# Kernel optimization log

Hardware: AMD Instinct MI355X
Metric: run time of the kernel (lower is better)

The kernel has to match this reference:

```python
import jax, jax.numpy as jnp
import numpy as np

B, C, H, W = 8, 512, 32, 32
NUM_HEADS = 8
HEAD_DIM = C // NUM_HEADS


def setup_inputs() -> dict:
    key = jax.random.key(0)
    k1, k2, k3 = jax.random.split(key, 3)
    query = jax.random.normal(k1, (B, C, H, W), dtype=jnp.float32)
    key_value = jax.random.normal(k2, (B, C, H, W), dtype=jnp.float32)
    # Linear(dim, 3*dim): store as [C, 3C] so y = x @ W + b
    W_qkv = jax.random.normal(k3, (C, 3 * C), dtype=jnp.float32) * (C ** -0.5)
    b_qkv = jnp.zeros((3 * C,), dtype=jnp.float32)
    return {"query": query, "key_value": key_value, "W_qkv": W_qkv, "b_qkv": b_qkv}


def reference(query, key_value, W_qkv, b_qkv):
    Bb, Cc, Hh, Ww = query.shape
    seq = Hh * Ww
    scale = HEAD_DIM ** -0.5

    # [B, C, H, W] -> [B, S, C]
    q_seq = query.reshape(Bb, Cc, seq).transpose(0, 2, 1)
    kv_seq = key_value.reshape(Bb, Cc, seq).transpose(0, 2, 1)

    # Original calls full qkv_proj and slices; math == projecting with sliced weights.
    q = q_seq @ W_qkv[:, :Cc] + b_qkv[:Cc]
    k = kv_seq @ W_qkv[:, Cc:2 * Cc] + b_qkv[Cc:2 * Cc]
    v = kv_seq @ W_qkv[:, 2 * Cc:] + b_qkv[2 * Cc:]

    def heads(x):  # [B, S, C] -> [B, nH, S, hd]
        return x.reshape(Bb, seq, NUM_HEADS, HEAD_DIM).transpose(0, 2, 1, 3)

    q, k, v = heads(q), heads(k), heads(v)
    attn = jnp.einsum('bhqd,bhkd->bhqk', q, k) * scale
    attn = jax.nn.softmax(attn, axis=-1)  # dropout: identity in eval
    out = jnp.einsum('bhqk,bhkd->bhqd', attn, v)
    # [B, nH, S, hd] -> [B, S, C] -> [B, C, H, W]
    out = out.transpose(0, 2, 1, 3).reshape(Bb, seq, Cc)
    return out.transpose(0, 2, 1).reshape(Bb, Cc, Hh, Ww)
```

## Files before the change

### kernel.cpp

```cpp
#include <hip/hip_runtime.h>
#include <hip/hip_bf16.h>

using short4v = __attribute__((ext_vector_type(4))) short;
using short8  = __attribute__((ext_vector_type(8))) short;
using uint2v  = __attribute__((ext_vector_type(2))) unsigned int;
using f32x4   = __attribute__((ext_vector_type(4))) float;

static constexpr int CDIM = 512;
static constexpr float KSCALE = 0.125f * 1.44269504088896341f;

__device__ __forceinline__ short f2bf(float f) {
  unsigned u = __builtin_bit_cast(unsigned, f);
  u = (u + 0x7fffu + ((u >> 16) & 1u)) >> 16;
  return (short)(unsigned short)u;
}
__device__ __forceinline__ unsigned pack_bf16(float a, float b) {
  return (unsigned)(unsigned short)f2bf(a) | ((unsigned)(unsigned short)f2bf(b) << 16);
}

#define GLOAD_LDS16(gp, lp)                                                              \
  __builtin_amdgcn_global_load_lds((const __attribute__((address_space(1))) void*)(gp),  \
                                   (__attribute__((address_space(3))) void*)(lp), 16, 0, 0)
#define MFMA16(a, b, c) __builtin_amdgcn_mfma_f32_16x16x32_bf16((a), (b), (c), 0, 0, 0)
#define WAIT_LGKM0() __builtin_amdgcn_s_waitcnt(0xc07f)

__global__ __launch_bounds__(256) void prep_transpose(const float* __restrict__ query,
                                                      const float* __restrict__ keyv,
                                                      const float* __restrict__ Wqkv,
                                                      short* __restrict__ Xq_t,
                                                      short* __restrict__ Xkv_t,
                                                      short* __restrict__ W_t) {
  __shared__ float tile[64 * 65];
  const int id = blockIdx.x;
  const float* s; short* d; int R, C, r0, c0;
  if (id < 2048) {
    const int which = id >> 10;
    int rem = id & 1023;
    const int b = rem >> 7; rem &= 127;
    R = 512; C = 1024;
    s = (which ? keyv : query) + (size_t)b * 512 * 1024;
    d = (which ? Xkv_t : Xq_t) + (size_t)b * 512 * 1024;
    r0 = (rem >> 4) * 64; c0 = (rem & 15) * 64;
  } else {
    const int rem = id - 2048;
    R = 512; C = 1536; s = Wqkv; d = W_t;
    r0 = (rem / 24) * 64; c0 = (rem % 24) * 64;
  }
  const int t  = threadIdx.x;
  const int rr = t >> 4;
  const int c4 = (t & 15) * 4;
#pragma unroll
  for (int i = 0; i < 4; ++i) {
    const int r = rr + i * 16;
    f32x4 v = *(const f32x4*)(s + (size_t)(r0 + r) * C + c0 + c4);
#pragma unroll
    for (int j = 0; j < 4; ++j) tile[(c4 + j) * 65 + r] = v[j];
  }
  __syncthreads();
  const int r8 = (t & 7) * 8;
#pragma unroll
  for (int i = 0; i < 2; ++i) {
    const int c = (t >> 3) + i * 32;
    short8 pk;
#pragma unroll
    for (int j = 0; j < 8; ++j) pk[j] = f2bf(tile[c * 65 + r8 + j]);
    *(short8*)(d + (size_t)(c0 + c) * R + r0 + r8) = pk;
  }
}

__global__ __launch_bounds__(256, 2) void qkv_gemm(const short* __restrict__ Xq,
                                                   const short* __restrict__ Xkv,
                                                   const short* __restrict__ Wt,
                                                   const float* __restrict__ bias,
                                                   short* __restrict__ Qg,
                                                   short* __restrict__ Kg,
                                                   short* __restrict__ Vt) {
  __shared__ short Asm[128 * 64];
  __shared__ short Bsm[256 * 64];
  __shared__ short epi[4 * 1152];
  const int id = blockIdx.x;
  const int n_blk = id >> 6;
  const int m_blk = ((id & 7) << 3) | ((id >> 3) & 7);
  const int n0 = n_blk << 8;
  const int m0 = m_blk << 7;
  const short* A = (n0 < CDIM) ? Xq : Xkv;
  const int t = threadIdx.x;
  const int w = t >> 6, l = t & 63;
  const int wm = w & 1, wn = w >> 1;
  const int lc = l & 15, lr = l >> 4;

  f32x4 acc[4][8];
#pragma unroll
  for (int i = 0; i < 4; ++i)
#pragma unroll
    for (int j = 0; j < 8; ++j) acc[i][j] = (f32x4){0.f, 0.f, 0.f, 0.f};

  for (int kb = 0; kb < 8; ++kb) {
    const int k0 = kb * 64;
#pragma unroll
    for (int i = 0; i < 4; ++i) {
      const int Qi = (w * 4 + i) * 64 + l;
      const int row = Qi >> 3, u = Qi & 7;
      GLOAD_LDS16(A + (size_t)(m0 + row) * CDIM + k0 + ((u ^ (row & 7)) * 8), &Asm[Qi * 8]);
    }
#pragma unroll
    for (int i = 0; i < 8; ++i) {
      const int Qi = (w * 8 + i) * 64 + l;
      const int row = Qi >> 3, u = Qi & 7;
      GLOAD_LDS16(Wt + (size_t)(n0 + row) * CDIM + k0 + ((u ^ (row & 7)) * 8), &Bsm[Qi * 8]);
    }
    __syncthreads();
#pragma unroll
    for (int kc = 0; kc < 2; ++kc) {
      short8 af[4], bfr[8];
#pragma unroll
      for (int mt = 0; mt < 4; ++mt) {
        const int row = wm * 64 + mt * 16 + lc;
        af[mt] = *(const short8*)(&Asm[(row * 8 + ((kc * 4 + lr) ^ (row & 7))) * 8]);
      }
#pragma unroll
      for (int nt = 0; nt < 8; ++nt) {
        const int row = wn * 128 + nt * 16 + lc;
        bfr[nt] = *(const short8*)(&Bsm[(row * 8 + ((kc * 4 + lr) ^ (row & 7))) * 8]);
      }
#pragma unroll
      for (int mt = 0; mt < 4; ++mt)
#pragma unroll
        for (int nt = 0; nt < 8; ++nt)
          acc[mt][nt] = MFMA16(af[mt], bfr[nt], acc[mt][nt]);
    }
    __syncthreads();
  }

  const int M0 = m0 + wm * 64;
  const int bb = M0 >> 10, s0 = M0 & 1023;
  const int N0 = n0 + wn * 128;
  float bv[8];
#pragma unroll
  for (int nt = 0; nt < 8; ++nt) bv[nt] = bias[N0 + nt * 16 + lc];
  short* slab = epi + w * 1152;

#pragma unroll
  for (int hi = 0; hi < 2; ++hi) {
    const int hg = (N0 >> 6) + hi;
    const int part = hg >> 3, hh = hg & 7;
    const int nb = hi * 4;
    if (part < 2) {
      const float osc = part ? 1.f : KSCALE;
      short* obase = (part ? Kg : Qg) + (size_t)(bb * 8 + hh) * 65536 + (size_t)s0 * 64;
#pragma unroll
      for (int mt = 0; mt < 4; ++mt) {
#pragma unroll
        for (int ntL = 0; ntL < 4; ++ntL)
#pragma unroll
          for (int r = 0; r < 4; ++r)
            slab[(lr * 4 + r) * 72 + ntL * 16 + lc] =
                f2bf((acc[mt][nb + ntL][r] + bv[nb + ntL]) * osc);
        WAIT_LGKM0();
#pragma unroll
        for (int i = 0; i < 2; ++i) {
          const int slot = i * 64 + l;
          const int m_l = slot >> 3, n8 = (slot & 7) * 8;
          short8 vv = *(const short8*)(&slab[m_l * 72 + n8]);
          *(short8*)(obase + (size_t)(mt * 16 + m_l) * 64 + n8) = vv;
        }
        WAIT_LGKM0();
      }
    } else {
      short* vbase = Vt + (size_t)(bb * 8 + hh) * 65536;
#pragma unroll
      for (int ntL = 0; ntL < 4; ++ntL) {
#pragma unroll
        for (int mt = 0; mt < 4; ++mt)
#pragma unroll
          for (int r = 0; r < 4; ++r)
            slab[lc * 72 + mt * 16 + lr * 4 + r] = f2bf(acc[mt][nb + ntL][r] + bv[nb + ntL]);
        WAIT_LGKM0();
#pragma unroll
        for (int i = 0; i < 2; ++i) {
          const int slot = i * 64 + l;
          const int dloc = slot >> 3, ch = (slot & 7) * 8;
          short8 vv = *(const short8*)(&slab[dloc * 72 + ch]);
          *(short8*)(vbase + (size_t)(ntL * 16 + dloc) * 1024 + s0 + ch) = vv;
        }
        WAIT_LGKM0();
      }
    }
  }
}

__global__ __launch_bounds__(256, 2) void flash_attn(const short* __restrict__ Qg,
                                                     const short* __restrict__ Kg,
                                                     const short* __restrict__ Vt,
                                                     float* __restrict__ out) {
  __shared__ alignas(16) short smem[25600];
  short* Ksm = smem;
  short* Vsm = smem + 8192;
  const int bh = blockIdx.x;
  const int b = bh >> 3, h = bh & 7;
  const int q0 = blockIdx.y * 128;
  const int t = threadIdx.x;
  const int w = t >> 6, l = t & 63;
  const int quad = l >> 4, l15 = l & 15;
  short* Pw = smem + 16384 + w * 2304;

  const short* Qbase = Qg + (size_t)bh * 65536;
  const short* Kbase = Kg + (size_t)bh * 65536;
  const short* Vbase = Vt + (size_t)bh * 65536;

  short8 bq[2][2];
#pragma unroll
  for (int qs = 0; qs < 2; ++qs) {
    const short* qrow = Qbase + (size_t)(q0 + qs * 64 + w * 16 + l15) * 64;
    bq[qs][0] = *(const short8*)(qrow + quad * 8);
    bq[qs][1] = *(const short8*)(qrow + 32 + quad * 8);
  }

  float lp[2] = {0.f, 0.f};
  f32x4 Oac[2][4];
#pragma unroll
  for (int qs = 0; qs < 2; ++qs)
#pragma unroll
    for (int dt = 0; dt < 4; ++dt) Oac[qs][dt] = (f32x4){0.f, 0.f, 0.f, 0.f};

  for (int it2 = 0; it2 < 8; ++it2) {
#pragma unroll
    for (int half = 0; half < 2; ++half) {
      const int kk0 = (it2 * 2 + half) * 64;
      short* Kd = Ksm + half * 4096;
      short* Vd = Vsm + half * 4096;
#pragma unroll
      for (int i = 0; i < 2; ++i) {
        const int Qi = (w * 2 + i) * 64 + l;
        const int sr = Qi >> 3, u = Qi & 7;
        GLOAD_LDS16(Kbase + (size_t)(kk0 + sr) * 64 + (u ^ (sr & 7)) * 8, &Kd[Qi * 8]);
        GLOAD_LDS16(Vbase + (size_t)sr * 1024 + kk0 + (u ^ (sr & 7)) * 8, &Vd[Qi * 8]);
      }
    }
    __syncthreads();

#pragma unroll
    for (int half = 0; half < 2; ++half) {
      const short* Kh = Ksm + half * 4096;
      const short* Vh = Vsm + half * 4096;
      short8 kf[2][4];
#pragma unroll
      for (int c = 0; c < 2; ++c)
#pragma unroll
        for (int nt = 0; nt < 4; ++nt) {
          const int srow = nt * 16 + l15;
          kf[c][nt] = *(const short8*)(&Kh[(srow * 8 + ((c * 4 + quad) ^ (srow & 7))) * 8]);
        }

#pragma unroll
      for (int qs = 0; qs < 2; ++qs) {
        f32x4 st[4];
#pragma unroll
        for (int nt = 0; nt < 4; ++nt) {
          st[nt] = (f32x4){0.f, 0.f, 0.f, 0.f};
#pragma unroll
          for (int c = 0; c < 2; ++c) st[nt] = MFMA16(kf[c][nt], bq[qs][c], st[nt]);
        }
        short* Ps = Pw + qs * 1152;
#pragma unroll
        for (int nt = 0; nt < 4; ++nt) {
          float p0 = __builtin_amdgcn_exp2f(st[nt][0]);
          float p1 = __builtin_amdgcn_exp2f(st[nt][1]);
          float p2 = __builtin_amdgcn_exp2f(st[nt][2]);
          float p3 = __builtin_amdgcn_exp2f(st[nt][3]);
          lp[qs] += (p0 + p1) + (p2 + p3);
          uint2v pk;
          pk[0] = pack_bf16(p0, p1);
          pk[1] = pack_bf16(p2, p3);
          *(short4v*)(&Ps[l15 * 72 + (nt * 4 + quad) * 4]) = __builtin_bit_cast(short4v, pk);
        }
      }
      WAIT_LGKM0();

#pragma unroll
      for (int c = 0; c < 2; ++c) {
        short8 pb0 = *(const short8*)(&Pw[l15 * 72 + (c * 8 + quad * 2) * 4]);
        short8 pb1 = *(const short8*)(&Pw[1152 + l15 * 72 + (c * 8 + quad * 2) * 4]);
#pragma unroll
        for (int dt = 0; dt < 4; ++dt) {
          const int drow = dt * 16 + l15;
          short8 vf = *(const short8*)(&Vh[(drow * 8 + ((c * 4 + quad) ^ (drow & 7))) * 8]);
          Oac[0][dt] = MFMA16(vf, pb0, Oac[0][dt]);
          Oac[1][dt] = MFMA16(vf, pb1, Oac[1][dt]);
        }
      }
      __syncthreads();
    }
  }

#pragma unroll
  for (int qs = 0; qs < 2; ++qs) {
    float lv = lp[qs];
    lv += __shfl_xor(lv, 16, 64);
    lv += __shfl_xor(lv, 32, 64);
    const float rinv = 1.f / lv;
    float* ob = out + ((size_t)(b * 512 + h * 64)) * 1024 + q0 + qs * 64 + w * 16 + l15;
#pragma unroll
    for (int dt = 0; dt < 4; ++dt)
#pragma unroll
      for (int r = 0; r < 4; ++r)
        ob[(size_t)(dt * 16 + quad * 4 + r) * 1024] = Oac[qs][dt][r] * rinv;
  }
}

extern "C" void kernel_launch(void* const* d_in, const int* in_sizes, int n_in,
                              void* d_out, int out_size, void* d_ws, size_t ws_size,
                              hipStream_t stream) {
  const float* query = (const float*)d_in[0];
  const float* keyv  = (const float*)d_in[1];
  const float* Wqkv  = (const float*)d_in[2];
  const float* bqkv  = (const float*)d_in[3];
  float* out = (float*)d_out;
  short* ws  = (short*)d_ws;

  short* Xq_t  = ws;
  short* Xkv_t = ws + 4194304;
  short* W_t   = ws + 8388608;
  short* Qg    = ws + 9175040;
  short* Kg    = ws + 13369344;
  short* Vt    = ws + 17563648;

  prep_transpose<<<dim3(2240), 256, 0, stream>>>(query, keyv, Wqkv, Xq_t, Xkv_t, W_t);
  qkv_gemm<<<dim3(384), 256, 0, stream>>>(Xq_t, Xkv_t, W_t, bqkv, Qg, Kg, Vt);
  flash_attn<<<dim3(64, 8, 1), 256, 0, stream>>>(Qg, Kg, Vt, out);
}
```

Baseline: 133.2 us.

## Fuse transpose, QKV GEMM and attention into one persistent kernel with grid barriers

Merges the three kernel launches into a single persistent kernel. Each block strides over the work items of each stage, and software grid barriers built on atomics separate the stages. The aim is to remove launch gaps and per-kernel tail effects. In exchange it adds a memset, host occupancy and device-property queries on every call, and spin-wait barriers. Stages lose their natural grid sizes (2240, 384 and 512 blocks become one occupancy-limited grid), and the barrier depends on all blocks being co-resident.

```diff
diff --git a/kernel.cpp b/kernel.cpp
--- a/kernel.cpp
+++ b/kernel.cpp
@@ -24,287 +24,307 @@
 #define MFMA16(a, b, c) __builtin_amdgcn_mfma_f32_16x16x32_bf16((a), (b), (c), 0, 0, 0)
 #define WAIT_LGKM0() __builtin_amdgcn_s_waitcnt(0xc07f)
 
-__global__ __launch_bounds__(256) void prep_transpose(const float* __restrict__ query,
-                                                      const float* __restrict__ keyv,
-                                                      const float* __restrict__ Wqkv,
-                                                      short* __restrict__ Xq_t,
-                                                      short* __restrict__ Xkv_t,
-                                                      short* __restrict__ W_t) {
-  __shared__ float tile[64 * 65];
-  const int id = blockIdx.x;
-  const float* s; short* d; int R, C, r0, c0;
-  if (id < 2048) {
-    const int which = id >> 10;
-    int rem = id & 1023;
-    const int b = rem >> 7; rem &= 127;
-    R = 512; C = 1024;
-    s = (which ? keyv : query) + (size_t)b * 512 * 1024;
-    d = (which ? Xkv_t : Xq_t) + (size_t)b * 512 * 1024;
-    r0 = (rem >> 4) * 64; c0 = (rem & 15) * 64;
-  } else {
-    const int rem = id - 2048;
-    R = 512; C = 1536; s = Wqkv; d = W_t;
-    r0 = (rem / 24) * 64; c0 = (rem % 24) * 64;
-  }
-  const int t  = threadIdx.x;
-  const int rr = t >> 4;
-  const int c4 = (t & 15) * 4;
-#pragma unroll
-  for (int i = 0; i < 4; ++i) {
-    const int r = rr + i * 16;
-    f32x4 v = *(const f32x4*)(s + (size_t)(r0 + r) * C + c0 + c4);
-#pragma unroll
-    for (int j = 0; j < 4; ++j) tile[(c4 + j) * 65 + r] = v[j];
+__device__ __forceinline__ void grid_barrier(unsigned* bar, unsigned nblk) {
+  __syncthreads();
+  if (threadIdx.x == 0) {
+    __threadfence();
+    atomicAdd(bar, 1u);
+    while (atomicAdd(bar, 0u) < nblk) __builtin_amdgcn_s_sleep(2);
+    __threadfence();
   }
   __syncthreads();
-  const int r8 = (t & 7) * 8;
-#pragma unroll
-  for (int i = 0; i < 2; ++i) {
-    const int c = (t >> 3) + i * 32;
-    short8 pk;
-#pragma unroll
-    for (int j = 0; j < 8; ++j) pk[j] = f2bf(tile[c * 65 + r8 + j]);
-    *(short8*)(d + (size_t)(c0 + c) * R + r0 + r8) = pk;
-  }
-}
-
-__global__ __launch_bounds__(256, 2) void qkv_gemm(const short* __restrict__ Xq,
-                                                   const short* __restrict__ Xkv,
-                                                   const short* __restrict__ Wt,
-                                                   const float* __restrict__ bias,
-                                                   short* __restrict__ Qg,
-                                                   short* __restrict__ Kg,
-                                                   short* __restrict__ Vt) {
-  __shared__ short Asm[128 * 64];
-  __shared__ short Bsm[256 * 64];
-  __shared__ short epi[4 * 1152];
-  const int id = blockIdx.x;
-  const int n_blk = id >> 6;
-  const int m_blk = ((id & 7) << 3) | ((id >> 3) & 7);
-  const int n0 = n_blk << 8;
-  const int m0 = m_blk << 7;
-  const short* A = (n0 < CDIM) ? Xq : Xkv;
+}
+
+__global__ __launch_bounds__(256, 2) void fused_attn(const float* __restrict__ query,
+                                                     const float* __restrict__ keyv,
+                                                     const float* __restrict__ Wqkv,
+                                                     const float* __restrict__ bqkv,
+                                                     short* __restrict__ Xq_t,
+                                                     short* __restrict__ Xkv_t,
+                                                     short* __restrict__ W_t,
+                                                     short* __restrict__ Qg,
+                                                     short* __restrict__ Kg,
+                                                     short* __restrict__ Vt,
+                                                     float* __restrict__ out,
+                                                     unsigned* __restrict__ bar,
+                                                     unsigned nblk) {
+  __shared__ __align__(16) char smem_raw[58368];
   const int t = threadIdx.x;
-  const int w = t >> 6, l = t & 63;
-  const int wm = w & 1, wn = w >> 1;
-  const int lc = l & 15, lr = l >> 4;
-
-  f32x4 acc[4][8];
-#pragma unroll
-  for (int i = 0; i < 4; ++i)
-#pragma unroll
-    for (int j = 0; j < 8; ++j) acc[i][j] = (f32x4){0.f, 0.f, 0.f, 0.f};
-
-  for (int kb = 0; kb < 8; ++kb) {
-    const int k0 = kb * 64;
-#pragma unroll
-    for (int i = 0; i < 4; ++i) {
-      const int Qi = (w * 4 + i) * 64 + l;
-      const int row = Qi >> 3, u = Qi & 7;
-      GLOAD_LDS16(A + (size_t)(m0 + row) * CDIM + k0 + ((u ^ (row & 7)) * 8), &Asm[Qi * 8]);
-    }
-#pragma unroll
-    for (int i = 0; i < 8; ++i) {
-      const int Qi = (w * 8 + i) * 64 + l;
-      const int row = Qi >> 3, u = Qi & 7;
-      GLOAD_LDS16(Wt + (size_t)(n0 + row) * CDIM + k0 + ((u ^ (row & 7)) * 8), &Bsm[Qi * 8]);
-    }
-    __syncthreads();
-#pragma unroll
-    for (int kc = 0; kc < 2; ++kc) {
-      short8 af[4], bfr[8];
-#pragma unroll
-      for (int mt = 0; mt < 4; ++mt) {
-        const int row = wm * 64 + mt * 16 + lc;
-        af[mt] = *(const short8*)(&Asm[(row * 8 + ((kc * 4 + lr) ^ (row & 7))) * 8]);
-      }
-#pragma unroll
-      for (int nt = 0; nt < 8; ++nt) {
-        const int row = wn * 128 + nt * 16 + lc;
-        bfr[nt] = *(const short8*)(&Bsm[(row * 8 + ((kc * 4 + lr) ^ (row & 7))) * 8]);
-      }
-#pragma unroll
-      for (int mt = 0; mt < 4; ++mt)
-#pragma unroll
-        for (int nt = 0; nt < 8; ++nt)
-          acc[mt][nt] = MFMA16(af[mt], bfr[nt], acc[mt][nt]);
-    }
-    __syncthreads();
-  }
-
-  const int M0 = m0 + wm * 64;
-  const int bb = M0 >> 10, s0 = M0 & 1023;
-  const int N0 = n0 + wn * 128;
-  float bv[8];
-#pragma unroll
-  for (int nt = 0; nt < 8; ++nt) bv[nt] = bias[N0 + nt * 16 + lc];
-  short* slab = epi + w * 1152;
-
-#pragma unroll
-  for (int hi = 0; hi < 2; ++hi) {
-    const int hg = (N0 >> 6) + hi;
-    const int part = hg >> 3, hh = hg & 7;
-    const int nb = hi * 4;
-    if (part < 2) {
-      const float osc = part ? 1.f : KSCALE;
-      short* obase = (part ? Kg : Qg) + (size_t)(bb * 8 + hh) * 65536 + (size_t)s0 * 64;
-#pragma unroll
-      for (int mt = 0; mt < 4; ++mt) {
-#pragma unroll
-        for (int ntL = 0; ntL < 4; ++ntL)
-#pragma unroll
-          for (int r = 0; r < 4; ++r)
-            slab[(lr * 4 + r) * 72 + ntL * 16 + lc] =
-                f2bf((acc[mt][nb + ntL][r] + bv[nb + ntL]) * osc);
-        WAIT_LGKM0();
-#pragma unroll
-        for (int i = 0; i < 2; ++i) {
-          const int slot = i * 64 + l;
-          const int m_l = slot >> 3, n8 = (slot & 7) * 8;
-          short8 vv = *(const short8*)(&slab[m_l * 72 + n8]);
-          *(short8*)(obase + (size_t)(mt * 16 + m_l) * 64 + n8) = vv;
-        }
-        WAIT_LGKM0();
-      }
-    } else {
-      short* vbase = Vt + (size_t)(bb * 8 + hh) * 65536;
-#pragma unroll
-      for (int ntL = 0; ntL < 4; ++ntL) {
-#pragma unroll
-        for (int mt = 0; mt < 4; ++mt)
-#pragma unroll
-          for (int r = 0; r < 4; ++r)
-            slab[lc * 72 + mt * 16 + lr * 4 + r] = f2bf(acc[mt][nb + ntL][r] + bv[nb + ntL]);
-        WAIT_LGKM0();
-#pragma unroll
-        for (int i = 0; i < 2; ++i) {
-          const int slot = i * 64 + l;
-          const int dloc = slot >> 3, ch = (slot & 7) * 8;
-          short8 vv = *(const short8*)(&slab[dloc * 72 + ch]);
-          *(short8*)(vbase + (size_t)(ntL * 16 + dloc) * 1024 + s0 + ch) = vv;
-        }
-        WAIT_LGKM0();
-      }
-    }
-  }
-}
-
-__global__ __launch_bounds__(256, 2) void flash_attn(const short* __restrict__ Qg,
-                                                     const short* __restrict__ Kg,
-                                                     const short* __restrict__ Vt,
-                                                     float* __restrict__ out) {
-  __shared__ alignas(16) short smem[25600];
-  short* Ksm = smem;
-  short* Vsm = smem + 8192;
-  const int bh = blockIdx.x;
-  const int b = bh >> 3, h = bh & 7;
-  const int q0 = blockIdx.y * 128;
-  const int t = threadIdx.x;
-  const int w = t >> 6, l = t & 63;
-  const int quad = l >> 4, l15 = l & 15;
-  short* Pw = smem + 16384 + w * 2304;
-
-  const short* Qbase = Qg + (size_t)bh * 65536;
-  const short* Kbase = Kg + (size_t)bh * 65536;
-  const short* Vbase = Vt + (size_t)bh * 65536;
-
-  short8 bq[2][2];
-#pragma unroll
-  for (int qs = 0; qs < 2; ++qs) {
-    const short* qrow = Qbase + (size_t)(q0 + qs * 64 + w * 16 + l15) * 64;
-    bq[qs][0] = *(const short8*)(qrow + quad * 8);
-    bq[qs][1] = *(const short8*)(qrow + 32 + quad * 8);
-  }
-
-  float lp[2] = {0.f, 0.f};
-  f32x4 Oac[2][4];
-#pragma unroll
-  for (int qs = 0; qs < 2; ++qs)
-#pragma unroll
-    for (int dt = 0; dt < 4; ++dt) Oac[qs][dt] = (f32x4){0.f, 0.f, 0.f, 0.f};
-
-  for (int it2 = 0; it2 < 8; ++it2) {
-#pragma unroll
-    for (int half = 0; half < 2; ++half) {
-      const int kk0 = (it2 * 2 + half) * 64;
-      short* Kd = Ksm + half * 4096;
-      short* Vd = Vsm + half * 4096;
+  const int grid = gridDim.x;
+
+  {
+    float* tile = (float*)smem_raw;
+    const int rr = t >> 4;
+    const int c4 = (t & 15) * 4;
+    const int r8 = (t & 7) * 8;
+    for (int id = blockIdx.x; id < 2240; id += grid) {
+      const float* s; short* d; int R, C, r0, c0;
+      if (id < 2048) {
+        const int which = id >> 10;
+        int rem = id & 1023;
+        const int b = rem >> 7; rem &= 127;
+        R = 512; C = 1024;
+        s = (which ? keyv : query) + (size_t)b * 512 * 1024;
+        d = (which ? Xkv_t : Xq_t) + (size_t)b * 512 * 1024;
+        r0 = (rem >> 4) * 64; c0 = (rem & 15) * 64;
+      } else {
+        const int rem = id - 2048;
+        R = 512; C = 1536; s = Wqkv; d = W_t;
+        r0 = (rem / 24) * 64; c0 = (rem % 24) * 64;
+      }
+#pragma unroll
+      for (int i = 0; i < 4; ++i) {
+        const int r = rr + i * 16;
+        f32x4 v = *(const f32x4*)(s + (size_t)(r0 + r) * C + c0 + c4);
+#pragma unroll
+        for (int j = 0; j < 4; ++j) tile[(c4 + j) * 65 + r] = v[j];
+      }
+      __syncthreads();
 #pragma unroll
       for (int i = 0; i < 2; ++i) {
-        const int Qi = (w * 2 + i) * 64 + l;
-        const int sr = Qi >> 3, u = Qi & 7;
-        GLOAD_LDS16(Kbase + (size_t)(kk0 + sr) * 64 + (u ^ (sr & 7)) * 8, &Kd[Qi * 8]);
-        GLOAD_LDS16(Vbase + (size_t)sr * 1024 + kk0 + (u ^ (sr & 7)) * 8, &Vd[Qi * 8]);
-      }
-    }
-    __syncthreads();
-
-#pragma unroll
-    for (int half = 0; half < 2; ++half) {
-      const short* Kh = Ksm + half * 4096;
-      const short* Vh = Vsm + half * 4096;
-      short8 kf[2][4];
-#pragma unroll
-      for (int c = 0; c < 2; ++c)
-#pragma unroll
-        for (int nt = 0; nt < 4; ++nt) {
-          const int srow = nt * 16 + l15;
-          kf[c][nt] = *(const short8*)(&Kh[(srow * 8 + ((c * 4 + quad) ^ (srow & 7))) * 8]);
-        }
-
-#pragma unroll
-      for (int qs = 0; qs < 2; ++qs) {
-        f32x4 st[4];
-#pragma unroll
-        for (int nt = 0; nt < 4; ++nt) {
-          st[nt] = (f32x4){0.f, 0.f, 0.f, 0.f};
-#pragma unroll
-          for (int c = 0; c < 2; ++c) st[nt] = MFMA16(kf[c][nt], bq[qs][c], st[nt]);
-        }
-        short* Ps = Pw + qs * 1152;
-#pragma unroll
-        for (int nt = 0; nt < 4; ++nt) {
-          float p0 = __builtin_amdgcn_exp2f(st[nt][0]);
-          float p1 = __builtin_amdgcn_exp2f(st[nt][1]);
-          float p2 = __builtin_amdgcn_exp2f(st[nt][2]);
-          float p3 = __builtin_amdgcn_exp2f(st[nt][3]);
-          lp[qs] += (p0 + p1) + (p2 + p3);
-          uint2v pk;
-          pk[0] = pack_bf16(p0, p1);
-          pk[1] = pack_bf16(p2, p3);
-          *(short4v*)(&Ps[l15 * 72 + (nt * 4 + quad) * 4]) = __builtin_bit_cast(short4v, pk);
-        }
-      }
-      WAIT_LGKM0();
-
-#pragma unroll
-      for (int c = 0; c < 2; ++c) {
-        short8 pb0 = *(const short8*)(&Pw[l15 * 72 + (c * 8 + quad * 2) * 4]);
-        short8 pb1 = *(const short8*)(&Pw[1152 + l15 * 72 + (c * 8 + quad * 2) * 4]);
-#pragma unroll
-        for (int dt = 0; dt < 4; ++dt) {
-          const int drow = dt * 16 + l15;
-          short8 vf = *(const short8*)(&Vh[(drow * 8 + ((c * 4 + quad) ^ (drow & 7))) * 8]);
-          Oac[0][dt] = MFMA16(vf, pb0, Oac[0][dt]);
-          Oac[1][dt] = MFMA16(vf, pb1, Oac[1][dt]);
-        }
+        const int c = (t >> 3) + i * 32;
+        short8 pk;
+#pragma unroll
+        for (int j = 0; j < 8; ++j) pk[j] = f2bf(tile[c * 65 + r8 + j]);
+        *(short8*)(d + (size_t)(c0 + c) * R + r0 + r8) = pk;
       }
       __syncthreads();
     }
   }
-
-#pragma unroll
-  for (int qs = 0; qs < 2; ++qs) {
-    float lv = lp[qs];
-    lv += __shfl_xor(lv, 16, 64);
-    lv += __shfl_xor(lv, 32, 64);
-    const float rinv = 1.f / lv;
-    float* ob = out + ((size_t)(b * 512 + h * 64)) * 1024 + q0 + qs * 64 + w * 16 + l15;
-#pragma unroll
-    for (int dt = 0; dt < 4; ++dt)
-#pragma unroll
-      for (int r = 0; r < 4; ++r)
-        ob[(size_t)(dt * 16 + quad * 4 + r) * 1024] = Oac[qs][dt][r] * rinv;
+  grid_barrier(&bar[0], nblk);
+
+  {
+    short* Asm = (short*)smem_raw;
+    short* Bsm = Asm + 8192;
+    short* epi = Bsm + 16384;
+    const int w = t >> 6, l = t & 63;
+    const int wm = w & 1, wn = w >> 1;
+    const int lc = l & 15, lr = l >> 4;
+    for (int id = blockIdx.x; id < 384; id += grid) {
+      const int n_blk = id >> 6;
+      const int m_blk = ((id & 7) << 3) | ((id >> 3) & 7);
+      const int n0 = n_blk << 8;
+      const int m0 = m_blk << 7;
+      const short* A = (n0 < CDIM) ? Xq_t : Xkv_t;
+
+      f32x4 acc[4][8];
+#pragma unroll
+      for (int i = 0; i < 4; ++i)
+#pragma unroll
+        for (int j = 0; j < 8; ++j) acc[i][j] = (f32x4){0.f, 0.f, 0.f, 0.f};
+
+      for (int kb = 0; kb < 8; ++kb) {
+        const int k0 = kb * 64;
+#pragma unroll
+        for (int i = 0; i < 4; ++i) {
+          const int Qi = (w * 4 + i) * 64 + l;
+          const int row = Qi >> 3, u = Qi & 7;
+          GLOAD_LDS16(A + (size_t)(m0 + row) * CDIM + k0 + ((u ^ (row & 7)) * 8), &Asm[Qi * 8]);
+        }
+#pragma unroll
+        for (int i = 0; i < 8; ++i) {
+          const int Qi = (w * 8 + i) * 64 + l;
+          const int row = Qi >> 3, u = Qi & 7;
+          GLOAD_LDS16(W_t + (size_t)(n0 + row) * CDIM + k0 + ((u ^ (row & 7)) * 8), &Bsm[Qi * 8]);
+        }
+        __syncthreads();
+#pragma unroll
+        for (int kc = 0; kc < 2; ++kc) {
+          short8 af[4], bfr[8];
+#pragma unroll
+          for (int mt = 0; mt < 4; ++mt) {
+            const int row = wm * 64 + mt * 16 + lc;
+            af[mt] = *(const short8*)(&Asm[(row * 8 + ((kc * 4 + lr) ^ (row & 7))) * 8]);
+          }
+#pragma unroll
+          for (int nt = 0; nt < 8; ++nt) {
+            const int row = wn * 128 + nt * 16 + lc;
+            bfr[nt] = *(const short8*)(&Bsm[(row * 8 + ((kc * 4 + lr) ^ (row & 7))) * 8]);
+          }
+#pragma unroll
+          for (int mt = 0; mt < 4; ++mt)
+#pragma unroll
+            for (int nt = 0; nt < 8; ++nt)
+              acc[mt][nt] = MFMA16(af[mt], bfr[nt], acc[mt][nt]);
+        }
+        __syncthreads();
+      }
+
+      const int M0 = m0 + wm * 64;
+      const int bb = M0 >> 10, s0 = M0 & 1023;
+      const int N0 = n0 + wn * 128;
+      float bv[8];
+#pragma unroll
+      for (int nt = 0; nt < 8; ++nt) bv[nt] = bqkv[N0 + nt * 16 + lc];
+      short* slab = epi + w * 1152;
+
+#pragma unroll
+      for (int hi = 0; hi < 2; ++hi) {
+        const int hg = (N0 >> 6) + hi;
+        const int part = hg >> 3, hh = hg & 7;
+        const int nb = hi * 4;
+        if (part < 2) {
+          const float osc = part ? 1.f : KSCALE;
+          short* obase = (part ? Kg : Qg) + (size_t)(bb * 8 + hh) * 65536 + (size_t)s0 * 64;
+#pragma unroll
+          for (int mt = 0; mt < 4; ++mt) {
+#pragma unroll
+            for (int ntL = 0; ntL < 4; ++ntL)
+#pragma unroll
+              for (int r = 0; r < 4; ++r)
+                slab[(lr * 4 + r) * 72 + ntL * 16 + lc] =
+                    f2bf((acc[mt][nb + ntL][r] + bv[nb + ntL]) * osc);
+            WAIT_LGKM0();
+#pragma unroll
+            for (int i = 0; i < 2; ++i) {
+              const int slot = i * 64 + l;
+              const int m_l = slot >> 3, n8 = (slot & 7) * 8;
+              short8 vv = *(const short8*)(&slab[m_l * 72 + n8]);
+              *(short8*)(obase + (size_t)(mt * 16 + m_l) * 64 + n8) = vv;
+            }
+            WAIT_LGKM0();
+          }
+        } else {
+          short* vbase = Vt + (size_t)(bb * 8 + hh) * 65536;
+#pragma unroll
+          for (int ntL = 0; ntL < 4; ++ntL) {
+#pragma unroll
+            for (int mt = 0; mt < 4; ++mt)
+#pragma unroll
+              for (int r = 0; r < 4; ++r)
+                slab[lc * 72 + mt * 16 + lr * 4 + r] = f2bf(acc[mt][nb + ntL][r] + bv[nb + ntL]);
+            WAIT_LGKM0();
+#pragma unroll
+            for (int i = 0; i < 2; ++i) {
+              const int slot = i * 64 + l;
+              const int dloc = slot >> 3, ch = (slot & 7) * 8;
+              short8 vv = *(const short8*)(&slab[dloc * 72 + ch]);
+              *(short8*)(vbase + (size_t)(ntL * 16 + dloc) * 1024 + s0 + ch) = vv;
+            }
+            WAIT_LGKM0();
+          }
+        }
+      }
+      __syncthreads();
+    }
+  }
+  grid_barrier(&bar[16], nblk);
+
+  {
+    short* smem = (short*)smem_raw;
+    short* Ksm = smem;
+    short* Vsm = smem + 8192;
+    const int w = t >> 6, l = t & 63;
+    const int quad = l >> 4, l15 = l & 15;
+    short* Pw = smem + 16384 + w * 2304;
+
+    for (int id = blockIdx.x; id < 512; id += grid) {
+      const int bh = id & 63;
+      const int b = bh >> 3, h = bh & 7;
+      const int q0 = (id >> 6) * 128;
+      const short* Qbase = Qg + (size_t)bh * 65536;
+      const short* Kbase = Kg + (size_t)bh * 65536;
+      const short* Vbase = Vt + (size_t)bh * 65536;
+
+      short8 bq[2][2];
+#pragma unroll
+      for (int qs = 0; qs < 2; ++qs) {
+        const short* qrow = Qbase + (size_t)(q0 + qs * 64 + w * 16 + l15) * 64;
+        bq[qs][0] = *(const short8*)(qrow + quad * 8);
+        bq[qs][1] = *(const short8*)(qrow + 32 + quad * 8);
+      }
+
+      float lp[2] = {0.f, 0.f};
+      f32x4 Oac[2][4];
+#pragma unroll
+      for (int qs = 0; qs < 2; ++qs)
+#pragma unroll
+        for (int dt = 0; dt < 4; ++dt) Oac[qs][dt] = (f32x4){0.f, 0.f, 0.f, 0.f};
+
+      for (int it2 = 0; it2 < 8; ++it2) {
+#pragma unroll
+        for (int half = 0; half < 2; ++half) {
+          const int kk0 = (it2 * 2 + half) * 64;
+          short* Kd = Ksm + half * 4096;
+          short* Vd = Vsm + half * 4096;
+#pragma unroll
+          for (int i = 0; i < 2; ++i) {
+            const int Qi = (w * 2 + i) * 64 + l;
+            const int sr = Qi >> 3, u = Qi & 7;
+            GLOAD_LDS16(Kbase + (size_t)(kk0 + sr) * 64 + (u ^ (sr & 7)) * 8, &Kd[Qi * 8]);
+            GLOAD_LDS16(Vbase + (size_t)sr * 1024 + kk0 + (u ^ (sr & 7)) * 8, &Vd[Qi * 8]);
+          }
+        }
+        __syncthreads();
+
+#pragma unroll
+        for (int half = 0; half < 2; ++half) {
+          const short* Kh = Ksm + half * 4096;
+          const short* Vh = Vsm + half * 4096;
+          short8 kf[2][4];
+#pragma unroll
+          for (int c = 0; c < 2; ++c)
+#pragma unroll
+            for (int nt = 0; nt < 4; ++nt) {
+              const int srow = nt * 16 + l15;
+              kf[c][nt] = *(const short8*)(&Kh[(srow * 8 + ((c * 4 + quad) ^ (srow & 7))) * 8]);
+            }
+
+#pragma unroll
+          for (int qs = 0; qs < 2; ++qs) {
+            f32x4 st[4];
+#pragma unroll
+            for (int nt = 0; nt < 4; ++nt) {
+              st[nt] = (f32x4){0.f, 0.f, 0.f, 0.f};
+#pragma unroll
+              for (int c = 0; c < 2; ++c) st[nt] = MFMA16(kf[c][nt], bq[qs][c], st[nt]);
+            }
+            short* Ps = Pw + qs * 1152;
+#pragma unroll
+            for (int nt = 0; nt < 4; ++nt) {
+              float p0 = __builtin_amdgcn_exp2f(st[nt][0]);
+              float p1 = __builtin_amdgcn_exp2f(st[nt][1]);
+              float p2 = __builtin_amdgcn_exp2f(st[nt][2]);
+              float p3 = __builtin_amdgcn_exp2f(st[nt][3]);
+              lp[qs] += (p0 + p1) + (p2 + p3);
+              uint2v pk;
+              pk[0] = pack_bf16(p0, p1);
+              pk[1] = pack_bf16(p2, p3);
+              *(short4v*)(&Ps[l15 * 72 + (nt * 4 + quad) * 4]) = __builtin_bit_cast(short4v, pk);
+            }
+          }
+          WAIT_LGKM0();
+
+#pragma unroll
+          for (int c = 0; c < 2; ++c) {
+            short8 pb0 = *(const short8*)(&Pw[l15 * 72 + (c * 8 + quad * 2) * 4]);
+            short8 pb1 = *(const short8*)(&Pw[1152 + l15 * 72 + (c * 8 + quad * 2) * 4]);
+#pragma unroll
+            for (int dt = 0; dt < 4; ++dt) {
+              const int drow = dt * 16 + l15;
+              short8 vf = *(const short8*)(&Vh[(drow * 8 + ((c * 4 + quad) ^ (drow & 7))) * 8]);
+              Oac[0][dt] = MFMA16(vf, pb0, Oac[0][dt]);
+              Oac[1][dt] = MFMA16(vf, pb1, Oac[1][dt]);
+            }
+          }
+          __syncthreads();
+        }
+      }
+
+#pragma unroll
+      for (int qs = 0; qs < 2; ++qs) {
+        float lv = lp[qs];
+        lv += __shfl_xor(lv, 16, 64);
+        lv += __shfl_xor(lv, 32, 64);
+        const float rinv = 1.f / lv;
+        float* ob = out + ((size_t)(b * 512 + h * 64)) * 1024 + q0 + qs * 64 + w * 16 + l15;
+#pragma unroll
+        for (int dt = 0; dt < 4; ++dt)
+#pragma unroll
+          for (int r = 0; r < 4; ++r)
+            ob[(size_t)(dt * 16 + quad * 4 + r) * 1024] = Oac[qs][dt][r] * rinv;
+      }
+    }
   }
 }
 
@@ -324,8 +344,20 @@
   short* Qg    = ws + 9175040;
   short* Kg    = ws + 13369344;
   short* Vt    = ws + 17563648;
-
-  prep_transpose<<<dim3(2240), 256, 0, stream>>>(query, keyv, Wqkv, Xq_t, Xkv_t, W_t);
-  qkv_gemm<<<dim3(384), 256, 0, stream>>>(Xq_t, Xkv_t, W_t, bqkv, Qg, Kg, Vt);
-  flash_attn<<<dim3(64, 8, 1), 256, 0, stream>>>(Qg, Kg, Vt, out);
-}
+  unsigned* bar = (unsigned*)((char*)d_ws + (64u << 20));
+
+  int occ = 0;
+  (void)hipOccupancyMaxActiveBlocksPerMultiprocessor(&occ, fused_attn, 256, 0);
+  hipDeviceProp_t prop;
+  int dev = 0;
+  (void)hipGetDevice(&dev);
+  (void)hipGetDeviceProperties(&prop, dev);
+  int grid = occ * prop.multiProcessorCount;
+  if (grid > 512) grid = 512;
+  if (grid < 1) grid = 1;
+
+  (void)hipMemsetAsync(bar, 0, 128, stream);
+  fused_attn<<<dim3(grid), dim3(256), 0, stream>>>(query, keyv, Wqkv, bqkv,
+                                                   Xq_t, Xkv_t, W_t, Qg, Kg, Vt, out,
+                                                   bar, (unsigned)grid);
+}
```

Result: slower. 207.4 us (+55.7%).
